# Kernel tuning notes

Measured on AMD Instinct MI355X. Metric: run time of the kernel, lower is better.

The kernel has to match this reference:

```python
import jax, jax.numpy as jnp
import numpy as np

N_HEAD, D_MODEL, D_K, D_V = 16, 1024, 64, 64
B, S = 4, 2048


def setup_inputs() -> dict:
    key = jax.random.key(0)
    ks = jax.random.split(key, 11)
    s = 0.02
    return {
        "q": jax.random.normal(ks[0], (B, S, D_MODEL), jnp.float32),
        "k": jax.random.normal(ks[1], (B, S, D_MODEL), jnp.float32),
        "v": jax.random.normal(ks[2], (B, S, D_MODEL), jnp.float32),
        "Wq": jax.random.normal(ks[3], (D_MODEL, N_HEAD * D_K), jnp.float32) * s,
        "bq": jnp.zeros((N_HEAD * D_K,), jnp.float32),
        "Wk": jax.random.normal(ks[4], (D_MODEL, N_HEAD * D_K), jnp.float32) * s,
        "bk": jnp.zeros((N_HEAD * D_K,), jnp.float32),
        "Wv": jax.random.normal(ks[5], (D_MODEL, N_HEAD * D_V), jnp.float32) * s,
        "bv": jnp.zeros((N_HEAD * D_V,), jnp.float32),
        "Wo": jax.random.normal(ks[6], (N_HEAD * D_V, D_MODEL), jnp.float32) * s,
        "bo": jnp.zeros((D_MODEL,), jnp.float32),
    }


def reference(q, k, v, Wq, bq, Wk, bk, Wv, bv, Wo, bo):
    b, s, _ = q.shape
    # project and split heads: [B,S,H,Dk] -> [B,H,S,Dk]
    qh = (q @ Wq + bq).reshape(b, s, N_HEAD, D_K).transpose(0, 2, 1, 3)
    kh = (k @ Wk + bk).reshape(b, s, N_HEAD, D_K).transpose(0, 2, 1, 3)
    vh = (v @ Wv + bv).reshape(b, s, N_HEAD, D_V).transpose(0, 2, 1, 3)
    scale = 1.0 / jnp.sqrt(jnp.float32(D_K))
    scores = jnp.einsum("bhqd,bhkd->bhqk", qh, kh) * scale  # [B,H,S,S]
    atten = jax.nn.softmax(scores, axis=-1)
    out = jnp.einsum("bhqk,bhkd->bhqd", atten, vh)  # [B,H,S,Dv]
    out = out.transpose(0, 2, 1, 3).reshape(b, s, N_HEAD * D_V)
    return out @ Wo + bo
```

## Files before the change

kernel.cpp:

```cpp
#include <hip/hip_runtime.h>

typedef unsigned short u16;
typedef __attribute__((ext_vector_type(4))) float f32x4;
typedef __attribute__((ext_vector_type(16))) float f32x16;
typedef __attribute__((ext_vector_type(8))) short bf16x8;
typedef __attribute__((ext_vector_type(4))) u16 u16x4;
typedef __attribute__((ext_vector_type(8))) u16 u16x8;

#define MFMA16(a, b, c) __builtin_amdgcn_mfma_f32_16x16x32_bf16((a), (b), (c), 0, 0, 0)
#define MFMA32(a, b, c) __builtin_amdgcn_mfma_f32_32x32x16_bf16((a), (b), (c), 0, 0, 0)

__device__ __forceinline__ u16 f2bf(float f) {
  union { float f; unsigned u; } x; x.f = f;
  unsigned r = x.u + 0x7fffu + ((x.u >> 16) & 1u);
  return (u16)(r >> 16);
}

__device__ __forceinline__ unsigned cvtpk(float lo, float hi) {
  unsigned r;
  asm("v_cvt_pk_bf16_f32 %0, %1, %2" : "=v"(r) : "v"(lo), "v"(hi));
  return r;
}

__device__ __forceinline__ void gl_lds16(const void* g, void* l) {
  __builtin_amdgcn_global_load_lds((const __attribute__((address_space(1))) void*)g,
                                   (__attribute__((address_space(3))) void*)l,
                                   16, 0, 0);
}

__global__ __launch_bounds__(256) void cvtT_k(const float* __restrict__ W0, const float* __restrict__ W1,
                                              const float* __restrict__ W2, const float* __restrict__ W3,
                                              u16* __restrict__ T0, u16* __restrict__ T1,
                                              u16* __restrict__ T2, u16* __restrict__ T3) {
  __shared__ u16 t[64][72];
  const float* W; u16* T;
  switch (blockIdx.z) {
    case 0: W = W0; T = T0; break;
    case 1: W = W1; T = T1; break;
    case 2: W = W2; T = T2; break;
    default: W = W3; T = T3; break;
  }
  const int tid = threadIdx.x;
  const int tr = blockIdx.x, tc = blockIdx.y;
#pragma unroll
  for (int i = 0; i < 4; ++i) {
    int row = i * 16 + (tid >> 4);
    int c4 = tid & 15;
    float4 v = *(const float4*)&W[(size_t)(tr * 64 + row) * 1024 + tc * 64 + c4 * 4];
    t[row][c4 * 4 + 0] = f2bf(v.x);
    t[row][c4 * 4 + 1] = f2bf(v.y);
    t[row][c4 * 4 + 2] = f2bf(v.z);
    t[row][c4 * 4 + 3] = f2bf(v.w);
  }
  __syncthreads();
#pragma unroll
  for (int i = 0; i < 4; ++i) {
    int orow = i * 16 + (tid >> 4);
    int occ = tid & 15;
    u16x4 o;
#pragma unroll
    for (int j = 0; j < 4; ++j) o[j] = t[occ * 4 + j][orow];
    *(u16x4*)&T[(size_t)(tc * 64 + orow) * 1024 + tr * 64 + occ * 4] = o;
  }
}

__global__ __launch_bounds__(512) void gemm_qkv_k(const float* __restrict__ Xq, const float* __restrict__ Xk,
                                                  const float* __restrict__ Xv, const u16* __restrict__ WTb,
                                                  const float* __restrict__ bq, const float* __restrict__ bk,
                                                  const float* __restrict__ bv,
                                                  u16* __restrict__ Qh, u16* __restrict__ Kh,
                                                  u16* __restrict__ Vt, float qscale) {
  __shared__ u16 As[2][128 * 64];
  __shared__ u16 Bs[3][128 * 64];
  const int tid = threadIdx.x;
  const int lane = tid & 63;
  const int w = tid >> 6;
  const int which = blockIdx.y >> 3;
  const int m0 = blockIdx.x * 128;
  const int n0 = (blockIdx.y & 7) * 128;
  const float* X = which == 0 ? Xq : (which == 1 ? Xk : Xv);
  const u16* WT = WTb + (size_t)which * 1024 * 1024;
  const float* bias = which == 0 ? bq : (which == 1 ? bk : bv);
  const int wr = (w >> 2) * 64;
  const int wc = (w & 3) * 32;
  const int l15 = lane & 15, l4 = lane >> 4, l7 = lane & 7;
  const int sr = lane >> 3;
  const int sc8 = ((lane & 7) ^ sr) * 8;
  const int arow = tid >> 3;
  const int ac = tid & 7;
  const int aswz = (ac ^ (arow & 7)) * 8;
  f32x4 acc[4][2] = {};
  float4 va_a[4], va_b[4];

#define BSTAGE(slot_, ks_) do {                                                              \
    int k0_ = (ks_) * 64;                                                                    \
    gl_lds16(WT + (size_t)(n0 + w * 16 + sr) * 1024 + k0_ + sc8, &Bs[slot_][(w * 16) * 64]);       \
    gl_lds16(WT + (size_t)(n0 + w * 16 + 8 + sr) * 1024 + k0_ + sc8, &Bs[slot_][(w * 16 + 8) * 64]); \
  } while (0)

#define ALOAD(VA, ks_) do {                                                                  \
    int k0_ = (ks_) * 64;                                                                    \
    VA[0] = *(const float4*)&X[(size_t)(m0 + arow) * 1024 + k0_ + ac * 8];                   \
    VA[1] = *(const float4*)&X[(size_t)(m0 + arow) * 1024 + k0_ + ac * 8 + 4];               \
    VA[2] = *(const float4*)&X[(size_t)(m0 + 64 + arow) * 1024 + k0_ + ac * 8];              \
    VA[3] = *(const float4*)&X[(size_t)(m0 + 64 + arow) * 1024 + k0_ + ac * 8 + 4];          \
  } while (0)

#define AWRITE(VA, slot_) do {                                                               \
    _Pragma("unroll")                                                                        \
    for (int i_ = 0; i_ < 2; ++i_) {                                                         \
      int row_ = i_ * 64 + arow;                                                             \
      const float4 vlo = VA[2 * i_], vhi = VA[2 * i_ + 1];                                   \
      union { unsigned u[4]; u16x8 v; } o_;                                                  \
      o_.u[0] = cvtpk(vlo.x, vlo.y); o_.u[1] = cvtpk(vlo.z, vlo.w);                          \
      o_.u[2] = cvtpk(vhi.x, vhi.y); o_.u[3] = cvtpk(vhi.z, vhi.w);                          \
      *(u16x8*)&As[slot_][row_ * 64 + aswz] = o_.v;                                          \
    }                                                                                        \
  } while (0)

#define COMPUTE(aslot_, bslot_) do {                                                         \
    const u16* Ac_ = As[aslot_];                                                             \
    const u16* Bc_ = Bs[bslot_];                                                             \
    _Pragma("unroll")                                                                        \
    for (int kk = 0; kk < 2; ++kk) {                                                         \
      int cs_ = ((kk * 4 + l4) ^ l7) * 8;                                                    \
      bf16x8 a_[4], b_[2];                                                                   \
      _Pragma("unroll")                                                                      \
      for (int t = 0; t < 4; ++t)                                                            \
        a_[t] = *(const bf16x8*)&Ac_[(wr + t * 16 + l15) * 64 + cs_];                        \
      _Pragma("unroll")                                                                      \
      for (int u = 0; u < 2; ++u)                                                            \
        b_[u] = *(const bf16x8*)&Bc_[(wc + u * 16 + l15) * 64 + cs_];                        \
      _Pragma("unroll")                                                                      \
      for (int mi = 0; mi < 4; ++mi)                                                         \
        _Pragma("unroll")                                                                    \
        for (int ni = 0; ni < 2; ++ni)                                                       \
          acc[mi][ni] = MFMA16(a_[mi], b_[ni], acc[mi][ni]);                                 \
    }                                                                                        \
  } while (0)

#define BODY(ks_, VA, DO_NEXT) do {                                                          \
    AWRITE(VA, (ks_) & 1);                                                                   \
    asm volatile("s_waitcnt lgkmcnt(0)" ::: "memory");                                       \
    asm volatile("s_waitcnt vmcnt(6)" ::: "memory");         \
    __builtin_amdgcn_s_barrier();                                                            \
    if (DO_NEXT) { BSTAGE(((ks_) + 2) % 3, (ks_) + 2); ALOAD(VA, (ks_) + 2); }               \
    __builtin_amdgcn_sched_barrier(0);                                                       \
    COMPUTE((ks_) & 1, (ks_) % 3);                                                           \
  } while (0)

  BSTAGE(0, 0);
  BSTAGE(1, 1);
  ALOAD(va_a, 0);
  ALOAD(va_b, 1);

  for (int i = 0; i < 7; ++i) {
    BODY(2 * i, va_a, 1);
    BODY(2 * i + 1, va_b, 1);
  }
  BODY(14, va_a, 0);
  BODY(15, va_b, 0);

#undef BSTAGE
#undef ALOAD
#undef AWRITE
#undef COMPUTE
#undef BODY

  const int lr = (lane >> 4) * 4;
  const int lc = lane & 15;
  if (which <= 1) {
    u16* ob = which == 0 ? Qh : Kh;
    float scale = which == 0 ? qscale : 1.0f;
#pragma unroll
    for (int mi = 0; mi < 4; ++mi)
#pragma unroll
      for (int ni = 0; ni < 2; ++ni) {
        int n = n0 + wc + ni * 16 + lc;
        float bb = bias[n];
        int h = n >> 6, d = n & 63;
#pragma unroll
        for (int r = 0; r < 4; ++r) {
          int m = m0 + wr + mi * 16 + lr + r;
          int b = m >> 11, s = m & 2047;
          ob[(((size_t)(b * 16 + h) * 2048 + s) << 6) + d] = f2bf((acc[mi][ni][r] + bb) * scale);
        }
      }
  } else {
#pragma unroll
    for (int mi = 0; mi < 4; ++mi)
#pragma unroll
      for (int ni = 0; ni < 2; ++ni) {
        int n = n0 + wc + ni * 16 + lc;
        float bb = bias[n];
        int h = n >> 6, d = n & 63;
        int m = m0 + wr + mi * 16 + lr;
        int b = m >> 11, s = m & 2047;
        u16x4 pk;
#pragma unroll
        for (int r = 0; r < 4; ++r) pk[r] = f2bf(acc[mi][ni][r] + bb);
        *(u16x4*)&Vt[((size_t)(b * 16 + h) * 64 + d) * 2048 + s] = pk;
      }
  }
}

__global__ __launch_bounds__(256) void gemm_o_k(const u16* __restrict__ X, const u16* __restrict__ WT,
                                                const float* __restrict__ bias, float* __restrict__ out) {
  __shared__ u16 As[128 * 64];
  __shared__ u16 Bs[128 * 64];
  const int tid = threadIdx.x;
  const int lane = tid & 63;
  const int w = tid >> 6;
  const int m0 = blockIdx.x * 128;
  const int n0 = blockIdx.y * 128;
  const int wr = (w >> 1) * 64;
  const int wc = (w & 1) * 64;
  const int l15 = lane & 15, l4 = lane >> 4, l7 = lane & 7;
  const int sr = lane >> 3;
  const int sc8 = ((lane & 7) ^ sr) * 8;
  f32x4 acc[4][4] = {};

  for (int ks = 0; ks < 16; ++ks) {
    const int k0 = ks * 64;
#pragma unroll
    for (int j = 0; j < 4; ++j) {
      int rb = w * 32 + j * 8;
      gl_lds16(X + (size_t)(m0 + rb + sr) * 1024 + k0 + sc8, &As[rb * 64]);
      gl_lds16(WT + (size_t)(n0 + rb + sr) * 1024 + k0 + sc8, &Bs[rb * 64]);
    }
    __syncthreads();
#pragma unroll
    for (int kk = 0; kk < 2; ++kk) {
      int cs = ((kk * 4 + l4) ^ l7) * 8;
      bf16x8 a[4], b[4];
#pragma unroll
      for (int t = 0; t < 4; ++t) {
        a[t] = *(const bf16x8*)&As[(wr + t * 16 + l15) * 64 + cs];
        b[t] = *(const bf16x8*)&Bs[(wc + t * 16 + l15) * 64 + cs];
      }
#pragma unroll
      for (int mi = 0; mi < 4; ++mi)
#pragma unroll
        for (int ni = 0; ni < 4; ++ni)
          acc[mi][ni] = MFMA16(a[mi], b[ni], acc[mi][ni]);
    }
    __syncthreads();
  }

  const int lr = (lane >> 4) * 4;
  const int lc = lane & 15;
#pragma unroll
  for (int mi = 0; mi < 4; ++mi)
#pragma unroll
    for (int ni = 0; ni < 4; ++ni) {
      int n = n0 + wc + ni * 16 + lc;
      float bb = bias[n];
#pragma unroll
      for (int r = 0; r < 4; ++r) {
        int m = m0 + wr + mi * 16 + lr + r;
        out[(size_t)m * 1024 + n] = acc[mi][ni][r] + bb;
      }
    }
}

__global__ __launch_bounds__(512) void attn_k(const u16* __restrict__ Qh, const u16* __restrict__ Kh,
                                              const u16* __restrict__ Vt, u16* __restrict__ AO) {
  __shared__ u16 SMEM[4 * 8192];
  const int lane = threadIdx.x & 63, w = threadIdx.x >> 6;
  const int hi = lane >> 5, q = lane & 31;

  const int id = blockIdx.x;
  const int bh = ((id >> 3) & 7) * 8 + (id & 7);
  const int qt = id >> 6;
  const int q0 = qt * 256 + w * 32;

  const u16* Qb = Qh + (size_t)bh * 2048 * 64;
  const u16* Kb = Kh + (size_t)bh * 2048 * 64;
  const u16* Vb = Vt + (size_t)bh * 64 * 2048;

  bf16x8 qf[4];
#pragma unroll
  for (int c = 0; c < 4; ++c)
    qf[c] = *(const bf16x8*)&Qb[(size_t)(q0 + q) * 64 + c * 16 + hi * 8];

  bf16x8 onesf;
#pragma unroll
  for (int i = 0; i < 8; ++i) onesf[i] = (short)0x3F80;

  f32x16 o0 = {}, o1 = {}, ol = {};
  const int lo8 = lane * 8;

  const int srowK = (w & 1) * 32 + q;
  const int sck = ((w >> 1) * 2 + hi) * 8;

#define STAGE(slot_, kt_) do {                                                       \
    int k0_ = (kt_) * 64;                                                            \
    gl_lds16(Kb + (size_t)(k0_ + srowK) * 64 + sck, &SMEM[(slot_) * 8192 + w * 512]);          \
    gl_lds16(Vb + (size_t)srowK * 2048 + k0_ + sck, &SMEM[(slot_) * 8192 + 4096 + w * 512]);   \
  } while (0)

  STAGE(0, 0);
  STAGE(1, 1);
  STAGE(2, 2);

  for (int kt = 0; kt < 32; ++kt) {
    if (kt < 30)       asm volatile("s_waitcnt vmcnt(4)" ::: "memory");
    else if (kt == 30) asm volatile("s_waitcnt vmcnt(2)" ::: "memory");
    else               asm volatile("s_waitcnt vmcnt(0)" ::: "memory");
    __builtin_amdgcn_s_barrier();
    if (kt <= 28) STAGE((kt + 3) & 3, kt + 3);
    __builtin_amdgcn_sched_barrier(0);

    const u16* Kc = &SMEM[(kt & 3) * 8192];
    const u16* Vc = Kc + 4096;

    f32x16 s0 = {}, s1 = {};
    __builtin_amdgcn_s_setprio(1);
#pragma unroll
    for (int c = 0; c < 4; ++c) {
      bf16x8 k0 = *(const bf16x8*)&Kc[(c * 2) * 512 + lo8];
      bf16x8 k1 = *(const bf16x8*)&Kc[(c * 2 + 1) * 512 + lo8];
      s0 = MFMA32(k0, qf[c], s0);
      s1 = MFMA32(k1, qf[c], s1);
    }
    __builtin_amdgcn_s_setprio(0);

#pragma unroll
    for (int i = 0; i < 16; ++i) {
      s0[i] = __builtin_exp2f(s0[i]);
      s1[i] = __builtin_exp2f(s1[i]);
    }

    __builtin_amdgcn_s_setprio(1);
#pragma unroll
    for (int t = 0; t < 4; ++t) {
      unsigned wA, wB, wC, wD;
      if (t == 0) { wA = cvtpk(s0[0], s0[1]); wB = cvtpk(s0[2], s0[3]); wC = cvtpk(s0[4], s0[5]); wD = cvtpk(s0[6], s0[7]); }
      else if (t == 1) { wA = cvtpk(s0[8], s0[9]); wB = cvtpk(s0[10], s0[11]); wC = cvtpk(s0[12], s0[13]); wD = cvtpk(s0[14], s0[15]); }
      else if (t == 2) { wA = cvtpk(s1[0], s1[1]); wB = cvtpk(s1[2], s1[3]); wC = cvtpk(s1[4], s1[5]); wD = cvtpk(s1[6], s1[7]); }
      else { wA = cvtpk(s1[8], s1[9]); wB = cvtpk(s1[10], s1[11]); wC = cvtpk(s1[12], s1[13]); wD = cvtpk(s1[14], s1[15]); }
      asm("v_permlane32_swap_b32 %0, %1" : "+v"(wA), "+v"(wC));
      asm("v_permlane32_swap_b32 %0, %1" : "+v"(wB), "+v"(wD));
      union { unsigned u[4]; bf16x8 v; } pf;
      pf.u[0] = wA; pf.u[1] = wB; pf.u[2] = wC; pf.u[3] = wD;
      bf16x8 v0 = *(const bf16x8*)&Vc[(t * 2) * 512 + lo8];
      bf16x8 v1 = *(const bf16x8*)&Vc[(t * 2 + 1) * 512 + lo8];
      o0 = MFMA32(v0, pf.v, o0);
      o1 = MFMA32(v1, pf.v, o1);
      ol = MFMA32(onesf, pf.v, ol);
    }
    __builtin_amdgcn_s_setprio(0);
  }
#undef STAGE

  __builtin_amdgcn_s_barrier();

  float inv = 1.0f / ol[0];
  u16* ep = SMEM + w * 2048;
#pragma unroll
  for (int g = 0; g < 2; ++g) {
    const f32x16 oo = g ? o1 : o0;
#pragma unroll
    for (int j = 0; j < 8; ++j) {
      int d = g * 32 + (j & 1) * 2 + ((j >> 1) & 1) * 8 + (j >> 2) * 16 + 4 * hi;
      unsigned pw = cvtpk(oo[2 * j] * inv, oo[2 * j + 1] * inv);
      *(unsigned*)&ep[q * 64 + ((d >> 3) ^ (q & 7)) * 8 + (d & 7)] = pw;
    }
  }
  asm volatile("s_waitcnt lgkmcnt(0)" ::: "memory");
  const int b = bh >> 4, h = bh & 15;
#pragma unroll
  for (int i = 0; i < 4; ++i) {
    int r = i * 8 + (lane >> 3), c = lane & 7;
    u16x8 vv = *(const u16x8*)&ep[r * 64 + ((c ^ (r & 7)) * 8)];
    size_t row = (size_t)b * 2048 + q0 + r;
    *(u16x8*)&AO[row * 1024 + h * 64 + c * 8] = vv;
  }
}

extern "C" void kernel_launch(void* const* d_in, const int* in_sizes, int n_in,
                              void* d_out, int out_size, void* d_ws, size_t ws_size,
                              hipStream_t stream) {
  const float* q  = (const float*)d_in[0];
  const float* k  = (const float*)d_in[1];
  const float* v  = (const float*)d_in[2];
  const float* Wq = (const float*)d_in[3];
  const float* bq = (const float*)d_in[4];
  const float* Wk = (const float*)d_in[5];
  const float* bk = (const float*)d_in[6];
  const float* Wv = (const float*)d_in[7];
  const float* bv = (const float*)d_in[8];
  const float* Wo = (const float*)d_in[9];
  const float* bo = (const float*)d_in[10];
  float* out = (float*)d_out;

  char* ws = (char*)d_ws;
  const size_t SZX = (size_t)8192 * 1024 * 2;
  const size_t SZW = (size_t)1024 * 1024 * 2;
  u16* AO  = (u16*)(ws);
  u16* WTq = (u16*)(ws + 3 * SZX);
  u16* WTk = (u16*)(ws + 3 * SZX + SZW);
  u16* WTv = (u16*)(ws + 3 * SZX + 2 * SZW);
  u16* WTo = (u16*)(ws + 3 * SZX + 3 * SZW);
  u16* Qh  = (u16*)(ws + 3 * SZX + 4 * SZW);
  u16* Kh  = (u16*)(ws + 4 * SZX + 4 * SZW);
  u16* Vt  = (u16*)(ws + 5 * SZX + 4 * SZW);

  cvtT_k<<<dim3(16, 16, 4), dim3(256), 0, stream>>>(Wq, Wk, Wv, Wo, WTq, WTk, WTv, WTo);

  gemm_qkv_k<<<dim3(64, 24), dim3(512), 0, stream>>>(q, k, v, WTq, bq, bk, bv, Qh, Kh, Vt,
                                                     0.125f * 1.4426950408889634f);

  attn_k<<<dim3(512), dim3(512), 0, stream>>>(Qh, Kh, Vt, AO);

  gemm_o_k<<<dim3(64, 8), dim3(256), 0, stream>>>(AO, WTo, bo, out);
}
```

Measured before the change: 195.7 us.

## Halve QKV GEMM K-tile to 32 to shrink LDS and registers for occupancy

Cuts the per-stage K depth of the QKV projection GEMM from 64 to 32. This halves the LDS buffers and the A-prefetch registers, doubles the number of pipeline iterations, and reworks the swizzle and load indexing to match. It also sets a launch-bounds occupancy hint so more blocks can be resident per CU. The cost is twice as many barriers and waits per K, with less MFMA work between them to hide latency.

```diff
diff --git a/kernel.cpp b/kernel.cpp
--- a/kernel.cpp
+++ b/kernel.cpp
@@ -64,14 +64,14 @@
   }
 }
 
-__global__ __launch_bounds__(512) void gemm_qkv_k(const float* __restrict__ Xq, const float* __restrict__ Xk,
-                                                  const float* __restrict__ Xv, const u16* __restrict__ WTb,
-                                                  const float* __restrict__ bq, const float* __restrict__ bk,
-                                                  const float* __restrict__ bv,
-                                                  u16* __restrict__ Qh, u16* __restrict__ Kh,
-                                                  u16* __restrict__ Vt, float qscale) {
-  __shared__ u16 As[2][128 * 64];
-  __shared__ u16 Bs[3][128 * 64];
+__global__ __launch_bounds__(512, 8) void gemm_qkv_k(const float* __restrict__ Xq, const float* __restrict__ Xk,
+                                                     const float* __restrict__ Xv, const u16* __restrict__ WTb,
+                                                     const float* __restrict__ bq, const float* __restrict__ bk,
+                                                     const float* __restrict__ bv,
+                                                     u16* __restrict__ Qh, u16* __restrict__ Kh,
+                                                     u16* __restrict__ Vt, float qscale) {
+  __shared__ u16 As[2][128 * 32];
+  __shared__ u16 Bs[3][128 * 32];
   const int tid = threadIdx.x;
   const int lane = tid & 63;
   const int w = tid >> 6;
@@ -83,66 +83,56 @@
   const float* bias = which == 0 ? bq : (which == 1 ? bk : bv);
   const int wr = (w >> 2) * 64;
   const int wc = (w & 3) * 32;
-  const int l15 = lane & 15, l4 = lane >> 4, l7 = lane & 7;
-  const int sr = lane >> 3;
-  const int sc8 = ((lane & 7) ^ sr) * 8;
-  const int arow = tid >> 3;
-  const int ac = tid & 7;
-  const int aswz = (ac ^ (arow & 7)) * 8;
+  const int l15 = lane & 15, l4 = lane >> 4;
+  const int cs = (l4 ^ ((l15 >> 1) & 3)) * 8;
+  const int arow = tid >> 2;
+  const int ac = tid & 3;
+  const int aswz = (ac ^ ((arow >> 1) & 3)) * 8;
+  const int brow = w * 16 + (lane >> 2);
+  const int bch = (lane & 3) ^ ((brow >> 1) & 3);
   f32x4 acc[4][2] = {};
-  float4 va_a[4], va_b[4];
+  float4 va_a[2], va_b[2];
 
 #define BSTAGE(slot_, ks_) do {                                                              \
-    int k0_ = (ks_) * 64;                                                                    \
-    gl_lds16(WT + (size_t)(n0 + w * 16 + sr) * 1024 + k0_ + sc8, &Bs[slot_][(w * 16) * 64]);       \
-    gl_lds16(WT + (size_t)(n0 + w * 16 + 8 + sr) * 1024 + k0_ + sc8, &Bs[slot_][(w * 16 + 8) * 64]); \
+    int k0_ = (ks_) * 32;                                                                    \
+    gl_lds16(WT + (size_t)(n0 + brow) * 1024 + k0_ + bch * 8, &Bs[slot_][(w * 16) * 32]);    \
   } while (0)
 
 #define ALOAD(VA, ks_) do {                                                                  \
-    int k0_ = (ks_) * 64;                                                                    \
+    int k0_ = (ks_) * 32;                                                                    \
     VA[0] = *(const float4*)&X[(size_t)(m0 + arow) * 1024 + k0_ + ac * 8];                   \
     VA[1] = *(const float4*)&X[(size_t)(m0 + arow) * 1024 + k0_ + ac * 8 + 4];               \
-    VA[2] = *(const float4*)&X[(size_t)(m0 + 64 + arow) * 1024 + k0_ + ac * 8];              \
-    VA[3] = *(const float4*)&X[(size_t)(m0 + 64 + arow) * 1024 + k0_ + ac * 8 + 4];          \
   } while (0)
 
 #define AWRITE(VA, slot_) do {                                                               \
-    _Pragma("unroll")                                                                        \
-    for (int i_ = 0; i_ < 2; ++i_) {                                                         \
-      int row_ = i_ * 64 + arow;                                                             \
-      const float4 vlo = VA[2 * i_], vhi = VA[2 * i_ + 1];                                   \
-      union { unsigned u[4]; u16x8 v; } o_;                                                  \
-      o_.u[0] = cvtpk(vlo.x, vlo.y); o_.u[1] = cvtpk(vlo.z, vlo.w);                          \
-      o_.u[2] = cvtpk(vhi.x, vhi.y); o_.u[3] = cvtpk(vhi.z, vhi.w);                          \
-      *(u16x8*)&As[slot_][row_ * 64 + aswz] = o_.v;                                          \
-    }                                                                                        \
+    const float4 vlo = VA[0], vhi = VA[1];                                                   \
+    union { unsigned u[4]; u16x8 v; } o_;                                                    \
+    o_.u[0] = cvtpk(vlo.x, vlo.y); o_.u[1] = cvtpk(vlo.z, vlo.w);                            \
+    o_.u[2] = cvtpk(vhi.x, vhi.y); o_.u[3] = cvtpk(vhi.z, vhi.w);                            \
+    *(u16x8*)&As[slot_][arow * 32 + aswz] = o_.v;                                            \
   } while (0)
 
 #define COMPUTE(aslot_, bslot_) do {                                                         \
     const u16* Ac_ = As[aslot_];                                                             \
     const u16* Bc_ = Bs[bslot_];                                                             \
+    bf16x8 a_[4], b_[2];                                                                     \
     _Pragma("unroll")                                                                        \
-    for (int kk = 0; kk < 2; ++kk) {                                                         \
-      int cs_ = ((kk * 4 + l4) ^ l7) * 8;                                                    \
-      bf16x8 a_[4], b_[2];                                                                   \
+    for (int t = 0; t < 4; ++t)                                                              \
+      a_[t] = *(const bf16x8*)&Ac_[(wr + t * 16 + l15) * 32 + cs];                           \
+    _Pragma("unroll")                                                                        \
+    for (int u = 0; u < 2; ++u)                                                              \
+      b_[u] = *(const bf16x8*)&Bc_[(wc + u * 16 + l15) * 32 + cs];                           \
+    _Pragma("unroll")                                                                        \
+    for (int mi = 0; mi < 4; ++mi)                                                           \
       _Pragma("unroll")                                                                      \
-      for (int t = 0; t < 4; ++t)                                                            \
-        a_[t] = *(const bf16x8*)&Ac_[(wr + t * 16 + l15) * 64 + cs_];                        \
-      _Pragma("unroll")                                                                      \
-      for (int u = 0; u < 2; ++u)                                                            \
-        b_[u] = *(const bf16x8*)&Bc_[(wc + u * 16 + l15) * 64 + cs_];                        \
-      _Pragma("unroll")                                                                      \
-      for (int mi = 0; mi < 4; ++mi)                                                         \
-        _Pragma("unroll")                                                                    \
-        for (int ni = 0; ni < 2; ++ni)                                                       \
-          acc[mi][ni] = MFMA16(a_[mi], b_[ni], acc[mi][ni]);                                 \
-    }                                                                                        \
+      for (int ni = 0; ni < 2; ++ni)                                                         \
+        acc[mi][ni] = MFMA16(a_[mi], b_[ni], acc[mi][ni]);                                   \
   } while (0)
 
 #define BODY(ks_, VA, DO_NEXT) do {                                                          \
     AWRITE(VA, (ks_) & 1);                                                                   \
     asm volatile("s_waitcnt lgkmcnt(0)" ::: "memory");                                       \
-    asm volatile("s_waitcnt vmcnt(6)" ::: "memory");         \
+    asm volatile("s_waitcnt vmcnt(3)" ::: "memory");   \
     __builtin_amdgcn_s_barrier();                                                            \
     if (DO_NEXT) { BSTAGE(((ks_) + 2) % 3, (ks_) + 2); ALOAD(VA, (ks_) + 2); }               \
     __builtin_amdgcn_sched_barrier(0);                                                       \
@@ -154,12 +144,12 @@
   ALOAD(va_a, 0);
   ALOAD(va_b, 1);
 
-  for (int i = 0; i < 7; ++i) {
+  for (int i = 0; i < 15; ++i) {
     BODY(2 * i, va_a, 1);
     BODY(2 * i + 1, va_b, 1);
   }
-  BODY(14, va_a, 0);
-  BODY(15, va_b, 0);
+  BODY(30, va_a, 0);
+  BODY(31, va_b, 0);
 
 #undef BSTAGE
 #undef ALOAD
```

Result: slower. 354.6 us (+81.2%).
